# Optimization experiments

Hardware: AMD Instinct MI355X
Metric: run time of the kernel (lower is better)

## Reference

```python
import jax, jax.numpy as jnp
import numpy as np

EPS = 1e-4

@jax.custom_vjp
def bin_active(x):
    # BinActive: sign forward, straight-through (hard-tanh) backward
    return jnp.sign(x)

def _ba_fwd(x):
    return jnp.sign(x), x

def _ba_bwd(x, g):
    return (g * (jnp.abs(x) <= 1.0).astype(g.dtype),)

bin_active.defvjp(_ba_fwd, _ba_bwd)

def norm_bin(x):
    # per-node mean/std (torch .std is unbiased, ddof=1) then binarize
    x = x - jnp.mean(x, axis=1, keepdims=True)
    x = x / (jnp.std(x, axis=1, ddof=1, keepdims=True) + EPS)
    return bin_active(x)

def bin_weight(W):
    # XNOR-style weight binarization: per-output-row scale * sign(W)
    alpha = jnp.mean(jnp.abs(W), axis=1, keepdims=True)
    return alpha * jnp.sign(W)

def bi_sage_conv(x_src, x_tgt, edge_index, W_l, W_r, b):
    # mean-aggregate source messages onto targets, then two binarized linears
    src, dst = edge_index[0], edge_index[1]
    n_tgt = x_tgt.shape[0]
    msg = x_src[src]                                             # [E, F] gather
    agg = jax.ops.segment_sum(msg, dst, num_segments=n_tgt)       # [n_tgt, F]
    cnt = jax.ops.segment_sum(jnp.ones((src.shape[0],), x_src.dtype), dst,
                              num_segments=n_tgt)
    agg = agg / jnp.maximum(cnt, 1.0)[:, None]
    out = agg @ bin_weight(W_l).T + x_tgt @ bin_weight(W_r).T + b
    return out


def setup_inputs() -> dict:
    key = jax.random.key(0)
    ks = jax.random.split(key, 10)
    N0, N1, B = 292864, 11264, 1024
    F_IN, F_HID, F_OUT = 602, 256, 41
    E1, E2 = 281600, 10240
    x = jax.random.normal(ks[0], (N0, F_IN), dtype=jnp.float32)
    # bipartite edges: row0 = source idx in [0, n_src), row1 = target idx in [0, n_tgt)
    ei1 = jnp.stack([jax.random.randint(ks[1], (E1,), 0, N0),
                     jax.random.randint(ks[2], (E1,), 0, N1)]).astype(jnp.int64)
    ei2 = jnp.stack([jax.random.randint(ks[3], (E2,), 0, N1),
                     jax.random.randint(ks[4], (E2,), 0, B)]).astype(jnp.int64)
    s1 = 0.1
    return {
        "x": x,
        "edge_index1": ei1,
        "edge_index2": ei2,
        "n1": N1,
        "n_batch": B,
        "W1_l": s1 * jax.random.normal(ks[5], (F_HID, F_IN), dtype=jnp.float32),
        "W1_r": s1 * jax.random.normal(ks[6], (F_HID, F_IN), dtype=jnp.float32),
        "b1": jnp.zeros((F_HID,), jnp.float32),
        "W2_l": s1 * jax.random.normal(ks[7], (F_OUT, F_HID), dtype=jnp.float32),
        "W2_r": s1 * jax.random.normal(ks[8], (F_OUT, F_HID), dtype=jnp.float32),
        "b2": jnp.zeros((F_OUT,), jnp.float32),
    }


def reference(x, edge_index1, edge_index2, n1, n_batch,
              W1_l, W1_r, b1, W2_l, W2_r, b2):
    # layer 1
    x_t = x[:n1]
    h = bi_sage_conv(norm_bin(x), norm_bin(x_t), edge_index1, W1_l, W1_r, b1)
    h = jax.nn.relu(h)  # dropout p=0.0 -> identity
    # layer 2
    h_t = h[:n_batch]
    out = bi_sage_conv(norm_bin(h), norm_bin(h_t), edge_index2, W2_l, W2_r, b2)
    return jax.nn.log_softmax(out, axis=-1)
```

## Files before the change

kernel.cpp:

```cpp
#include <hip/hip_runtime.h>
#include <hip/hip_bf16.h>
#include <cstdint>
#include <cstddef>

#define CDIV(a,b) (((a)+(b)-1)/(b))

using bf16x8 = __attribute__((ext_vector_type(8))) short;
using f32x4  = __attribute__((ext_vector_type(4))) float;

struct __align__(8) F4 { float x, y, z, w; };
struct __align__(8) F2 { float x, y; };

__device__ __forceinline__ unsigned short sgn_bf16(float s){
  return (s > 0.f) ? 0x3F80u : ((s < 0.f) ? 0xBF80u : 0u);
}

__device__ __forceinline__ int colX(int k){
  int w = k >> 5, b = k & 31;
  if (w < 16){
    int g = w >> 3, wr = w & 7;
    int j = wr >> 1, half = wr & 1;
    return 256*g + 4*(32*half + b) + j;
  }
  int j = w - 16;
  int c = 512 + 4*b + j;
  return (c < 602) ? c : -1;
}
__device__ __forceinline__ int colH(int k){
  int w = k >> 5, b = k & 31;
  int j = w >> 1, half = w & 1;
  return 4*(32*half + b) + j;
}

__device__ __forceinline__ void pack_row602(F4 v0, F4 v1, F4 v2, int lane, uint32_t* pr){
  float s = v0.x+v0.y+v0.z+v0.w + v1.x+v1.y+v1.z+v1.w + v2.x+v2.y+v2.z+v2.w;
  #pragma unroll
  for (int off = 32; off; off >>= 1) s += __shfl_xor(s, off);
  const float mean = s / 602.f;
  uint32_t wpos[20], wneg[20];
  {
    float d0 = v0.x - mean, d1v = v0.y - mean, d2v = v0.z - mean, d3 = v0.w - mean;
    unsigned long long b0 = __ballot(d0 > 0.f), b1 = __ballot(d1v > 0.f),
                       b2 = __ballot(d2v > 0.f), b3 = __ballot(d3 > 0.f);
    wpos[0]=(uint32_t)b0; wpos[1]=(uint32_t)(b0>>32); wpos[2]=(uint32_t)b1; wpos[3]=(uint32_t)(b1>>32);
    wpos[4]=(uint32_t)b2; wpos[5]=(uint32_t)(b2>>32); wpos[6]=(uint32_t)b3; wpos[7]=(uint32_t)(b3>>32);
    b0 = __ballot(d0 < 0.f); b1 = __ballot(d1v < 0.f); b2 = __ballot(d2v < 0.f); b3 = __ballot(d3 < 0.f);
    wneg[0]=(uint32_t)b0; wneg[1]=(uint32_t)(b0>>32); wneg[2]=(uint32_t)b1; wneg[3]=(uint32_t)(b1>>32);
    wneg[4]=(uint32_t)b2; wneg[5]=(uint32_t)(b2>>32); wneg[6]=(uint32_t)b3; wneg[7]=(uint32_t)(b3>>32);
  }
  {
    float d0 = v1.x - mean, d1v = v1.y - mean, d2v = v1.z - mean, d3 = v1.w - mean;
    unsigned long long b0 = __ballot(d0 > 0.f), b1 = __ballot(d1v > 0.f),
                       b2 = __ballot(d2v > 0.f), b3 = __ballot(d3 > 0.f);
    wpos[8]=(uint32_t)b0; wpos[9]=(uint32_t)(b0>>32); wpos[10]=(uint32_t)b1; wpos[11]=(uint32_t)(b1>>32);
    wpos[12]=(uint32_t)b2; wpos[13]=(uint32_t)(b2>>32); wpos[14]=(uint32_t)b3; wpos[15]=(uint32_t)(b3>>32);
    b0 = __ballot(d0 < 0.f); b1 = __ballot(d1v < 0.f); b2 = __ballot(d2v < 0.f); b3 = __ballot(d3 < 0.f);
    wneg[8]=(uint32_t)b0; wneg[9]=(uint32_t)(b0>>32); wneg[10]=(uint32_t)b1; wneg[11]=(uint32_t)(b1>>32);
    wneg[12]=(uint32_t)b2; wneg[13]=(uint32_t)(b2>>32); wneg[14]=(uint32_t)b3; wneg[15]=(uint32_t)(b3>>32);
  }
  {
    int base = 4*lane;
    float d0 = v2.x - mean, d1v = v2.y - mean, d2v = v2.z - mean, d3 = v2.w - mean;
    wpos[16] = (uint32_t)__ballot((base+0 < 90) && (d0 > 0.f));
    wpos[17] = (uint32_t)__ballot((base+1 < 90) && (d1v > 0.f));
    wpos[18] = (uint32_t)__ballot((base+2 < 90) && (d2v > 0.f));
    wpos[19] = (uint32_t)__ballot((base+3 < 90) && (d3 > 0.f));
    wneg[16] = (uint32_t)__ballot((base+0 < 90) && (d0 < 0.f));
    wneg[17] = (uint32_t)__ballot((base+1 < 90) && (d1v < 0.f));
    wneg[18] = (uint32_t)__ballot((base+2 < 90) && (d2v < 0.f));
    wneg[19] = (uint32_t)__ballot((base+3 < 90) && (d3 < 0.f));
  }
  if (lane == 0){
    #pragma unroll
    for (int q = 0; q < 5; ++q){
      uint4 a; a.x = wpos[4*q]; a.y = wpos[4*q+1]; a.z = wpos[4*q+2]; a.w = wpos[4*q+3];
      *(uint4*)&pr[4*q] = a;
      uint4 b; b.x = wneg[4*q]; b.y = wneg[4*q+1]; b.z = wneg[4*q+2]; b.w = wneg[4*q+3];
      *(uint4*)&pr[20 + 4*q] = b;
    }
  }
}

__global__ void prep_all(const float* __restrict__ W1l, const float* __restrict__ W1r,
                         const float* __restrict__ W2l, const float* __restrict__ W2r,
                         float* __restrict__ aL, float* __restrict__ aR,
                         float* __restrict__ a2L, float* __restrict__ a2R,
                         int* __restrict__ degB, int ndeg,
                         unsigned short* __restrict__ bsgn,
                         unsigned char* __restrict__ mask, int n0, int n1){
  int r = blockIdx.x;
  if (r < 594){
    const float* wr; float* dst; int K;
    if (r < 256){ wr = W1l + (size_t)r*602; dst = aL + r; K = 602; }
    else if (r < 512){ int q = r-256; wr = W1r + (size_t)q*602; dst = aR + q; K = 602; }
    else if (r < 553){ int q = r-512; wr = W2l + (size_t)q*256; dst = a2L + q; K = 256; }
    else { int q = r-553; wr = W2r + (size_t)q*256; dst = a2R + q; K = 256; }
    float s = 0.f;
    for (int k = threadIdx.x; k < K; k += blockDim.x) s += fabsf(wr[k]);
    #pragma unroll
    for (int off = 32; off; off >>= 1) s += __shfl_xor(s, off);
    __shared__ float red[4];
    int wid = threadIdx.x >> 6, lane = threadIdx.x & 63;
    if (lane == 0) red[wid] = s;
    __syncthreads();
    if (threadIdx.x == 0) *dst = (red[0]+red[1]+red[2]+red[3]) / (float)K;
  } else if (r < 642){
    int i = (r - 594)*256 + threadIdx.x;
    if (i < ndeg) degB[i] = 0;
  } else if (r < 1922){
    int idx = (r - 642)*256 + threadIdx.x;
    if (idx < 256*1280){
      int o = idx / 1280, k = idx - o*1280;
      float v = 0.f;
      if (k < 640){ int c = colX(k);       if (c >= 0) v = W1l[(size_t)o*602 + c]; }
      else        { int c = colX(k - 640); if (c >= 0) v = W1r[(size_t)o*602 + c]; }
      bsgn[idx] = sgn_bf16(v);
    }
  } else {
    int i = (r - 1922)*256 + threadIdx.x;
    if (i < n0) mask[i] = (i < n1) ? 1 : 0;
  }
}

__global__ void mark_count(const int* __restrict__ s1, const int* __restrict__ d1, int E1,
                           unsigned char* __restrict__ mask, int* __restrict__ deg1,
                           const int* __restrict__ d2, int E2, int* __restrict__ deg2){
  int e = blockIdx.x*blockDim.x + threadIdx.x;
  if (e < E1){
    mask[s1[e]] = 1;
    atomicAdd(&deg1[d1[e]], 1);
  } else if (e < E1 + E2){
    atomicAdd(&deg2[d2[e - E1]], 1);
  }
}

__global__ void pack_scan_bcat(const float* __restrict__ X, uint32_t* __restrict__ P, int nrows,
                               const unsigned char* __restrict__ mask, int packBlocks,
                               const int* __restrict__ deg1, int* __restrict__ rs1, int* __restrict__ cur1, int n1c,
                               const int* __restrict__ deg2, int* __restrict__ rs2, int* __restrict__ cur2, int n2c,
                               const float* __restrict__ W2l, const float* __restrict__ W2r,
                               const float* __restrict__ a2L, const float* __restrict__ a2R,
                               float* __restrict__ Bcat2){
  __shared__ int partial[256];
  const int bid = blockIdx.x;
  if (bid >= packBlocks){
    int role = bid - packBlocks;
    if (role < 2){
      const int* deg = role ? deg2 : deg1;
      int* rs  = role ? rs2  : rs1;
      int* cur = role ? cur2 : cur1;
      int n    = role ? n2c  : n1c;
      int tid = threadIdx.x;
      int per = CDIV(n, 256);
      int begin = tid*per; if (begin > n) begin = n;
      int end = begin + per; if (end > n) end = n;
      int s = 0;
      for (int i = begin; i < end; ++i) s += deg[i];
      partial[tid] = s;
      __syncthreads();
      for (int off = 1; off < 256; off <<= 1){
        int add = (tid >= off) ? partial[tid-off] : 0;
        __syncthreads();
        partial[tid] += add;
        __syncthreads();
      }
      int prefix = (tid == 0) ? 0 : partial[tid-1];
      for (int i = begin; i < end; ++i){ rs[i] = prefix; cur[i] = prefix; prefix += deg[i]; }
      if (tid == 255) rs[n] = prefix;
    } else {
      int idx = (role - 2)*256 + threadIdx.x;
      if (idx < 512*41){
        int o = idx % 41, k = idx / 41;
        int c = (k < 256) ? colH(k) : colH(k - 256);
        float w = (k < 256) ? W2l[(size_t)o*256 + c] : W2r[(size_t)o*256 + c];
        float a = (k < 256) ? a2L[o] : a2R[o];
        float sg = (w > 0.f) ? 1.f : ((w < 0.f) ? -1.f : 0.f);
        Bcat2[idx] = a * sg;
      }
    }
    return;
  }
  const int rp = bid*4 + (threadIdx.x >> 6);
  const int lane = threadIdx.x & 63;
  const int rowA = rp*2, rowB = rp*2 + 1;
  if (rowA >= nrows) return;
  const bool mA = mask[rowA] != 0;
  const bool mB = (rowB < nrows) && (mask[rowB] != 0);
  if (!mA && !mB) return;
  F4 a0 = {0.f,0.f,0.f,0.f}, a1 = a0, a2 = a0;
  F4 c0 = a0, c1 = a0, c2 = a0;
  const float* xa = X + (size_t)rowA * 602;
  const float* xb = X + (size_t)rowB * 602;
  if (mA){
    a0 = *(const F4*)&xa[4*lane];
    a1 = *(const F4*)&xa[256 + 4*lane];
    if (lane < 22) a2 = *(const F4*)&xa[512 + 4*lane];
    else if (lane == 22){ F2 t = *(const F2*)&xa[600]; a2.x = t.x; a2.y = t.y; }
  }
  if (mB){
    c0 = *(const F4*)&xb[4*lane];
    c1 = *(const F4*)&xb[256 + 4*lane];
    if (lane < 22) c2 = *(const F4*)&xb[512 + 4*lane];
    else if (lane == 22){ F2 t = *(const F2*)&xb[600]; c2.x = t.x; c2.y = t.y; }
  }
  if (mA) pack_row602(a0, a1, a2, lane, P + (size_t)rowA * 40);
  if (mB) pack_row602(c0, c1, c2, lane, P + (size_t)rowB * 40);
}

__global__ void fill_both(const int* __restrict__ s1, const int* __restrict__ d1, int E1,
                          int* __restrict__ cur1, int* __restrict__ esrc1,
                          const int* __restrict__ s2, const int* __restrict__ d2, int E2,
                          int* __restrict__ cur2, int* __restrict__ esrc2){
  int e = blockIdx.x*blockDim.x + threadIdx.x;
  if (e < E1){
    int p = atomicAdd(&cur1[d1[e]], 1);
    esrc1[p] = s1[e];
  } else if (e < E1 + E2){
    int q = e - E1;
    int p = atomicAdd(&cur2[d2[q]], 1);
    esrc2[p] = s2[q];
  }
}

__global__ void aggregate_v3(const uint32_t* __restrict__ packed,
                             const int* __restrict__ rs, const int* __restrict__ esrc,
                             unsigned short* __restrict__ S, float* __restrict__ invdeg){
  const int t = blockIdx.x;
  const int lane = threadIdx.x;
  const int slot = lane / 20;
  const int w = lane - slot*20;
  const int s0 = rs[t], s1 = rs[t+1];
  const bool active = slot < 3;
  uint32_t p[8] = {0,0,0,0,0,0,0,0};
  uint32_t n[8] = {0,0,0,0,0,0,0,0};
  for (int base = s0; base < s1; base += 3){
    int e = base + slot;
    uint32_t wp = 0, wn = 0;
    if (active && e < s1){
      const uint32_t* pr = packed + (size_t)esrc[e] * 40;
      wp = pr[w];
      wn = pr[20 + w];
    }
    #pragma unroll
    for (int b = 0; b < 8; ++b){
      p[b] += (wp >> b) & 0x01010101u;
      n[b] += (wn >> b) & 0x01010101u;
    }
  }
  #pragma unroll
  for (int b = 0; b < 8; ++b){
    p[b] += __shfl(p[b], lane + 20) + __shfl(p[b], lane + 40);
    n[b] += __shfl(n[b], lane + 20) + __shfl(n[b], lane + 40);
  }
  if (lane == 0){
    int deg = s1 - s0;
    invdeg[t] = 1.f / (float)(deg > 0 ? deg : 1);
  }
  if (lane < 20){
    unsigned short* sr = S + (size_t)t * 640;
    #pragma unroll
    for (int b = 0; b < 8; ++b){
      #pragma unroll
      for (int k = 0; k < 4; ++k){
        int col = 32*lane + b + 8*k;
        int cnt = (int)((p[b] >> (8*k)) & 0xFF) - (int)((n[b] >> (8*k)) & 0xFF);
        float f = (float)cnt;
        sr[col] = (unsigned short)(__float_as_uint(f) >> 16);
      }
    }
  }
}

__global__ __launch_bounds__(256) void gemm1_fused(
    const unsigned short* __restrict__ Sx, const uint32_t* __restrict__ packedX,
    const unsigned short* __restrict__ bsgn, const float* __restrict__ invdeg,
    const float* __restrict__ aL, const float* __restrict__ aR,
    const float* __restrict__ bias, uint32_t* __restrict__ packedH){
  __shared__ __align__(16) char smem[33792];
  unsigned short (*As)[40] = (unsigned short (*)[40])smem;
  unsigned short (*Bs)[40] = (unsigned short (*)[40])(smem + 32*40*2);
  float (*Hs)[264] = (float (*)[264])smem;

  const int tid = threadIdx.x;
  const int lane = tid & 63, wid = tid >> 6;
  const int m0 = blockIdx.x * 32;
  const int frow = lane & 15, fk = (lane >> 4) * 8;
  const int sRow = tid >> 3, sK = (tid & 7) * 4;

  f32x4 acc1[2][4], acc2[2][4];
  #pragma unroll
  for (int i = 0; i < 2; ++i)
    #pragma unroll
    for (int j = 0; j < 4; ++j){ f32x4 z = {0.f,0.f,0.f,0.f}; acc1[i][j] = z; acc2[i][j] = z; }

  const unsigned short* SxRow = Sx + (size_t)(m0 + sRow) * 640;
  const uint32_t* pxRow = packedX + (size_t)(m0 + sRow) * 40;
  const unsigned short* bsgnCol = bsgn + (size_t)tid * 1280;

  for (int kc = 0; kc < 640; kc += 32){
    *(uint2*)&As[sRow][sK] = *(const uint2*)&SxRow[kc + sK];
    *(bf16x8*)&Bs[tid][0]  = *(const bf16x8*)&bsgnCol[kc];
    *(bf16x8*)&Bs[tid][8]  = *(const bf16x8*)&bsgnCol[kc + 8];
    *(bf16x8*)&Bs[tid][16] = *(const bf16x8*)&bsgnCol[kc + 16];
    *(bf16x8*)&Bs[tid][24] = *(const bf16x8*)&bsgnCol[kc + 24];
    __syncthreads();
    bf16x8 a0 = *(bf16x8*)&As[frow][fk];
    bf16x8 a1 = *(bf16x8*)&As[16 + frow][fk];
    #pragma unroll
    for (int nf = 0; nf < 4; ++nf){
      bf16x8 b = *(bf16x8*)&Bs[wid*64 + nf*16 + frow][fk];
      acc1[0][nf] = __builtin_amdgcn_mfma_f32_16x16x32_bf16(a0, b, acc1[0][nf], 0, 0, 0);
      acc1[1][nf] = __builtin_amdgcn_mfma_f32_16x16x32_bf16(a1, b, acc1[1][nf], 0, 0, 0);
    }
    __syncthreads();
  }
  for (int kc = 0; kc < 640; kc += 32){
    int w = kc >> 5;
    {
      uint32_t wp = pxRow[w];
      uint32_t wq = pxRow[20 + w];
      union { unsigned short u[4]; uint2 v; } tmp;
      #pragma unroll
      for (int j = 0; j < 4; ++j){
        int b_ = sK + j;
        tmp.u[j] = ((wp >> b_) & 1) ? 0x3F80u : (((wq >> b_) & 1) ? 0xBF80u : 0u);
      }
      *(uint2*)&As[sRow][sK] = tmp.v;
    }
    *(bf16x8*)&Bs[tid][0]  = *(const bf16x8*)&bsgnCol[640 + kc];
    *(bf16x8*)&Bs[tid][8]  = *(const bf16x8*)&bsgnCol[640 + kc + 8];
    *(bf16x8*)&Bs[tid][16] = *(const bf16x8*)&bsgnCol[640 + kc + 16];
    *(bf16x8*)&Bs[tid][24] = *(const bf16x8*)&bsgnCol[640 + kc + 24];
    __syncthreads();
    bf16x8 a0 = *(bf16x8*)&As[frow][fk];
    bf16x8 a1 = *(bf16x8*)&As[16 + frow][fk];
    #pragma unroll
    for (int nf = 0; nf < 4; ++nf){
      bf16x8 b = *(bf16x8*)&Bs[wid*64 + nf*16 + frow][fk];
      acc2[0][nf] = __builtin_amdgcn_mfma_f32_16x16x32_bf16(a0, b, acc2[0][nf], 0, 0, 0);
      acc2[1][nf] = __builtin_amdgcn_mfma_f32_16x16x32_bf16(a1, b, acc2[1][nf], 0, 0, 0);
    }
    __syncthreads();
  }

  #pragma unroll
  for (int nf = 0; nf < 4; ++nf){
    int gc = wid*64 + nf*16 + frow;
    float al = aL[gc], ar = aR[gc], bb = bias[gc];
    #pragma unroll
    for (int mf = 0; mf < 2; ++mf){
      #pragma unroll
      for (int reg = 0; reg < 4; ++reg){
        int lr = mf*16 + (lane >> 4)*4 + reg;
        float v = invdeg[m0 + lr]*al*acc1[mf][nf][reg] + ar*acc2[mf][nf][reg] + bb;
        Hs[lr][gc] = fmaxf(v, 0.f);
      }
    }
  }
  __syncthreads();

  for (int r = 0; r < 8; ++r){
    int row = wid*8 + r;
    float4 v = *(const float4*)&Hs[row][4*lane];
    float s = v.x + v.y + v.z + v.w;
    #pragma unroll
    for (int off = 32; off; off >>= 1) s += __shfl_xor(s, off);
    float mean = s * (1.f/256.f);
    float d0 = v.x - mean, d1v = v.y - mean, d2v = v.z - mean, d3 = v.w - mean;
    unsigned long long b0 = __ballot(d0 > 0.f), b1 = __ballot(d1v > 0.f),
                       b2 = __ballot(d2v > 0.f), b3 = __ballot(d3 > 0.f);
    uint32_t wpos[8], wneg[8];
    wpos[0]=(uint32_t)b0; wpos[1]=(uint32_t)(b0>>32); wpos[2]=(uint32_t)b1; wpos[3]=(uint32_t)(b1>>32);
    wpos[4]=(uint32_t)b2; wpos[5]=(uint32_t)(b2>>32); wpos[6]=(uint32_t)b3; wpos[7]=(uint32_t)(b3>>32);
    b0 = __ballot(d0 < 0.f); b1 = __ballot(d1v < 0.f); b2 = __ballot(d2v < 0.f); b3 = __ballot(d3 < 0.f);
    wneg[0]=(uint32_t)b0; wneg[1]=(uint32_t)(b0>>32); wneg[2]=(uint32_t)b1; wneg[3]=(uint32_t)(b1>>32);
    wneg[4]=(uint32_t)b2; wneg[5]=(uint32_t)(b2>>32); wneg[6]=(uint32_t)b3; wneg[7]=(uint32_t)(b3>>32);
    if (lane == 0){
      uint32_t* pr = packedH + (size_t)(m0 + row) * 16;
      *(uint4*)&pr[0]  = make_uint4(wpos[0], wpos[1], wpos[2], wpos[3]);
      *(uint4*)&pr[4]  = make_uint4(wpos[4], wpos[5], wpos[6], wpos[7]);
      *(uint4*)&pr[8]  = make_uint4(wneg[0], wneg[1], wneg[2], wneg[3]);
      *(uint4*)&pr[12] = make_uint4(wneg[4], wneg[5], wneg[6], wneg[7]);
    }
  }
}

__global__ void agg_gemm2(const uint32_t* __restrict__ packedH,
                          const int* __restrict__ rs, const int* __restrict__ esrc,
                          const float* __restrict__ Bcat2, const float* __restrict__ bias,
                          float* __restrict__ out){
  const int t = blockIdx.x;
  const int lane = threadIdx.x;
  const int slot = lane >> 3, w = lane & 7;
  __shared__ float av[512];
  const int s0 = rs[t], s1 = rs[t+1];
  uint32_t p[8] = {0,0,0,0,0,0,0,0};
  uint32_t n[8] = {0,0,0,0,0,0,0,0};
  for (int base = s0; base < s1; base += 8){
    int e = base + slot;
    uint32_t wp = 0, wn = 0;
    if (e < s1){
      const uint32_t* pr = packedH + (size_t)esrc[e] * 16;
      wp = pr[w];
      wn = pr[8 + w];
    }
    #pragma unroll
    for (int b = 0; b < 8; ++b){
      p[b] += (wp >> b) & 0x01010101u;
      n[b] += (wn >> b) & 0x01010101u;
    }
  }
  #pragma unroll
  for (int b = 0; b < 8; ++b){
    p[b] += __shfl_xor(p[b], 8);  p[b] += __shfl_xor(p[b], 16);  p[b] += __shfl_xor(p[b], 32);
    n[b] += __shfl_xor(n[b], 8);  n[b] += __shfl_xor(n[b], 16);  n[b] += __shfl_xor(n[b], 32);
  }
  int deg = s1 - s0;
  float inv = 1.f / (float)(deg > 0 ? deg : 1);
  if (lane < 8){
    #pragma unroll
    for (int b = 0; b < 8; ++b){
      #pragma unroll
      for (int k = 0; k < 4; ++k){
        int col = 32*lane + b + 8*k;
        int cnt = (int)((p[b] >> (8*k)) & 0xFF) - (int)((n[b] >> (8*k)) & 0xFF);
        av[col] = (float)cnt * inv;
      }
    }
  }
  const uint32_t* pr = packedH + (size_t)t * 16;
  for (int k = lane; k < 256; k += 64){
    int wq = k >> 5, b = k & 31;
    av[256 + k] = (float)((pr[wq] >> b) & 1) - (float)((pr[8 + wq] >> b) & 1);
  }
  __syncthreads();
  bool activeO = lane < 41;
  float acc = activeO ? bias[lane] : 0.f;
  for (int k = 0; k < 512; ++k){
    float bw = activeO ? Bcat2[k*41 + lane] : 0.f;
    acc += av[k] * bw;
  }
  float v = activeO ? acc : -INFINITY;
  float m = v;
  #pragma unroll
  for (int off = 32; off; off >>= 1) m = fmaxf(m, __shfl_xor(m, off));
  float e = activeO ? expf(v - m) : 0.f;
  float ssum = e;
  #pragma unroll
  for (int off = 32; off; off >>= 1) ssum += __shfl_xor(ssum, off);
  if (activeO) out[(size_t)t*41 + lane] = v - m - logf(ssum);
}

extern "C" void kernel_launch(void* const* d_in, const int* in_sizes, int n_in,
                              void* d_out, int out_size, void* d_ws, size_t ws_size,
                              hipStream_t stream){
  (void)n_in; (void)out_size; (void)ws_size;
  const float* x   = (const float*)d_in[0];
  const int*   ei1 = (const int*)d_in[1];
  const int*   ei2 = (const int*)d_in[2];
  const float* W1l = (const float*)d_in[5];
  const float* W1r = (const float*)d_in[6];
  const float* b1  = (const float*)d_in[7];
  const float* W2l = (const float*)d_in[8];
  const float* W2r = (const float*)d_in[9];
  const float* b2  = (const float*)d_in[10];
  float* out = (float*)d_out;

  const int FIN = 602, N1 = 11264, NB = 1024;
  const int N0 = in_sizes[0] / FIN;
  const int E1 = in_sizes[1] / 2;
  const int E2 = in_sizes[2] / 2;

  char* wsb = (char*)d_ws;
  size_t off = 0;
  auto carve = [&](size_t bytes)->void*{
    void* p = wsb + off;
    off = (off + bytes + 255) & ~(size_t)255;
    return p;
  };
  uint32_t* packedX = (uint32_t*)carve((size_t)N0*40*4);
  uint32_t* packedH = (uint32_t*)carve((size_t)N1*16*4);
  unsigned short* Sx = (unsigned short*)carve((size_t)N1*640*2);
  float* invdeg1 = (float*)carve((size_t)N1*4);
  unsigned short* bsgn = (unsigned short*)carve((size_t)256*1280*2);
  float* Bcat2 = (float*)carve((size_t)512*41*4);
  float* aL  = (float*)carve(256*4);
  float* aR  = (float*)carve(256*4);
  float* a2L = (float*)carve(64*4);
  float* a2R = (float*)carve(64*4);
  unsigned char* mask = (unsigned char*)carve((size_t)N0);
  int* degB  = (int*)carve((size_t)(N1+NB)*4);
  int* deg1  = degB;
  int* deg2  = degB + N1;
  int* rs1   = (int*)carve((size_t)(N1+1)*4);
  int* cur1  = (int*)carve((size_t)N1*4);
  int* esrc1 = (int*)carve((size_t)E1*4);
  int* rs2   = (int*)carve((size_t)(NB+1)*4);
  int* cur2  = (int*)carve((size_t)NB*4);
  int* esrc2 = (int*)carve((size_t)E2*4);

  const int maskBlocks = CDIV(N0, 256);
  const int cntBlocks  = CDIV(E1 + E2, 256);
  const int packBlocks = CDIV(N0, 8);
  const int bcatBlocks = CDIV(512*41, 256);

  prep_all<<<1922 + maskBlocks, 256, 0, stream>>>(
      W1l, W1r, W2l, W2r, aL, aR, a2L, a2R, degB, N1 + NB, bsgn, mask, N0, N1);
  mark_count<<<cntBlocks, 256, 0, stream>>>(ei1, ei1 + E1, E1, mask, deg1,
                                            ei2 + E2, E2, deg2);
  pack_scan_bcat<<<packBlocks + 2 + bcatBlocks, 256, 0, stream>>>(
      x, packedX, N0, mask, packBlocks,
      deg1, rs1, cur1, N1, deg2, rs2, cur2, NB,
      W2l, W2r, a2L, a2R, Bcat2);
  fill_both<<<cntBlocks, 256, 0, stream>>>(ei1, ei1 + E1, E1, cur1, esrc1,
                                           ei2, ei2 + E2, E2, cur2, esrc2);
  aggregate_v3<<<N1, 64, 0, stream>>>(packedX, rs1, esrc1, Sx, invdeg1);
  gemm1_fused<<<N1/32, 256, 0, stream>>>(Sx, packedX, bsgn, invdeg1, aL, aR, b1, packedH);
  agg_gemm2<<<NB, 64, 0, stream>>>(packedH, rs2, esrc2, Bcat2, b2, out);
}
```

Before: 270.7 us.

## Merge prep and edge-count kernels, memset buffers, register-prefetch GEMM tiles

Folds the edge marking and degree counting into the weight-prep kernel, so one launch does both. The mask and degree buffers are now zeroed with async memsets instead of kernel blocks. The first n1 rows are treated as masked directly in the pack kernel. In gemm1, the next k-chunk of the global A and B operands is loaded into registers before the current chunk's MFMAs run, so global latency overlaps compute. The extra prefetch registers may lower occupancy.

```diff
diff --git a/kernel.cpp b/kernel.cpp
--- a/kernel.cpp
+++ b/kernel.cpp
@@ -81,13 +81,14 @@
   }
 }
 
-__global__ void prep_all(const float* __restrict__ W1l, const float* __restrict__ W1r,
-                         const float* __restrict__ W2l, const float* __restrict__ W2r,
-                         float* __restrict__ aL, float* __restrict__ aR,
-                         float* __restrict__ a2L, float* __restrict__ a2R,
-                         int* __restrict__ degB, int ndeg,
-                         unsigned short* __restrict__ bsgn,
-                         unsigned char* __restrict__ mask, int n0, int n1){
+__global__ void prep_mark(const float* __restrict__ W1l, const float* __restrict__ W1r,
+                          const float* __restrict__ W2l, const float* __restrict__ W2r,
+                          float* __restrict__ aL, float* __restrict__ aR,
+                          float* __restrict__ a2L, float* __restrict__ a2R,
+                          unsigned short* __restrict__ bsgn,
+                          const int* __restrict__ ei1, int E1,
+                          unsigned char* __restrict__ mask, int* __restrict__ deg1,
+                          const int* __restrict__ ei2, int E2, int* __restrict__ deg2){
   int r = blockIdx.x;
   if (r < 594){
     const float* wr; float* dst; int K;
@@ -104,33 +105,22 @@
     if (lane == 0) red[wid] = s;
     __syncthreads();
     if (threadIdx.x == 0) *dst = (red[0]+red[1]+red[2]+red[3]) / (float)K;
-  } else if (r < 642){
-    int i = (r - 594)*256 + threadIdx.x;
-    if (i < ndeg) degB[i] = 0;
-  } else if (r < 1922){
-    int idx = (r - 642)*256 + threadIdx.x;
-    if (idx < 256*1280){
-      int o = idx / 1280, k = idx - o*1280;
-      float v = 0.f;
-      if (k < 640){ int c = colX(k);       if (c >= 0) v = W1l[(size_t)o*602 + c]; }
-      else        { int c = colX(k - 640); if (c >= 0) v = W1r[(size_t)o*602 + c]; }
-      bsgn[idx] = sgn_bf16(v);
-    }
+  } else if (r < 1874){
+    int idx = (r - 594)*256 + threadIdx.x;
+    int o = idx / 1280, k = idx - o*1280;
+    float v = 0.f;
+    if (k < 640){ int c = colX(k);       if (c >= 0) v = W1l[(size_t)o*602 + c]; }
+    else        { int c = colX(k - 640); if (c >= 0) v = W1r[(size_t)o*602 + c]; }
+    bsgn[idx] = sgn_bf16(v);
   } else {
-    int i = (r - 1922)*256 + threadIdx.x;
-    if (i < n0) mask[i] = (i < n1) ? 1 : 0;
-  }
-}
-
-__global__ void mark_count(const int* __restrict__ s1, const int* __restrict__ d1, int E1,
-                           unsigned char* __restrict__ mask, int* __restrict__ deg1,
-                           const int* __restrict__ d2, int E2, int* __restrict__ deg2){
-  int e = blockIdx.x*blockDim.x + threadIdx.x;
-  if (e < E1){
-    mask[s1[e]] = 1;
-    atomicAdd(&deg1[d1[e]], 1);
-  } else if (e < E1 + E2){
-    atomicAdd(&deg2[d2[e - E1]], 1);
+    int e = (r - 1874)*256 + threadIdx.x;
+    if (e < E1){
+      mask[ei1[e]] = 1;
+      atomicAdd(&deg1[ei1[E1 + e]], 1);
+    } else if (e < E1 + E2){
+      int q = e - E1;
+      atomicAdd(&deg2[ei2[E2 + q]], 1);
+    }
   }
 }
 
@@ -184,8 +174,8 @@
   const int lane = threadIdx.x & 63;
   const int rowA = rp*2, rowB = rp*2 + 1;
   if (rowA >= nrows) return;
-  const bool mA = mask[rowA] != 0;
-  const bool mB = (rowB < nrows) && (mask[rowB] != 0);
+  const bool mA = (rowA < n1c) || (mask[rowA] != 0);
+  const bool mB = (rowB < nrows) && ((rowB < n1c) || (mask[rowB] != 0));
   if (!mA && !mB) return;
   F4 a0 = {0.f,0.f,0.f,0.f}, a1 = a0, a2 = a0;
   F4 c0 = a0, c1 = a0, c2 = a0;
@@ -297,13 +287,37 @@
   const uint32_t* pxRow = packedX + (size_t)(m0 + sRow) * 40;
   const unsigned short* bsgnCol = bsgn + (size_t)tid * 1280;
 
+  bf16x8 pb0, pb1, pb2, pb3;
+  uint2 pa;
+  uint32_t pw0 = 0, pw1 = 0;
+
+  pb0 = *(const bf16x8*)&bsgnCol[0];
+  pb1 = *(const bf16x8*)&bsgnCol[8];
+  pb2 = *(const bf16x8*)&bsgnCol[16];
+  pb3 = *(const bf16x8*)&bsgnCol[24];
+  pa  = *(const uint2*)&SxRow[sK];
+
   for (int kc = 0; kc < 640; kc += 32){
-    *(uint2*)&As[sRow][sK] = *(const uint2*)&SxRow[kc + sK];
-    *(bf16x8*)&Bs[tid][0]  = *(const bf16x8*)&bsgnCol[kc];
-    *(bf16x8*)&Bs[tid][8]  = *(const bf16x8*)&bsgnCol[kc + 8];
-    *(bf16x8*)&Bs[tid][16] = *(const bf16x8*)&bsgnCol[kc + 16];
-    *(bf16x8*)&Bs[tid][24] = *(const bf16x8*)&bsgnCol[kc + 24];
+    *(uint2*)&As[sRow][sK] = pa;
+    *(bf16x8*)&Bs[tid][0]  = pb0;
+    *(bf16x8*)&Bs[tid][8]  = pb1;
+    *(bf16x8*)&Bs[tid][16] = pb2;
+    *(bf16x8*)&Bs[tid][24] = pb3;
     __syncthreads();
+    int kn = kc + 32;
+    if (kn < 640){
+      pb0 = *(const bf16x8*)&bsgnCol[kn];
+      pb1 = *(const bf16x8*)&bsgnCol[kn + 8];
+      pb2 = *(const bf16x8*)&bsgnCol[kn + 16];
+      pb3 = *(const bf16x8*)&bsgnCol[kn + 24];
+      pa  = *(const uint2*)&SxRow[kn + sK];
+    } else {
+      pb0 = *(const bf16x8*)&bsgnCol[640];
+      pb1 = *(const bf16x8*)&bsgnCol[648];
+      pb2 = *(const bf16x8*)&bsgnCol[656];
+      pb3 = *(const bf16x8*)&bsgnCol[664];
+      pw0 = pxRow[0]; pw1 = pxRow[20];
+    }
     bf16x8 a0 = *(bf16x8*)&As[frow][fk];
     bf16x8 a1 = *(bf16x8*)&As[16 + frow][fk];
     #pragma unroll
@@ -315,23 +329,29 @@
     __syncthreads();
   }
   for (int kc = 0; kc < 640; kc += 32){
-    int w = kc >> 5;
     {
-      uint32_t wp = pxRow[w];
-      uint32_t wq = pxRow[20 + w];
       union { unsigned short u[4]; uint2 v; } tmp;
       #pragma unroll
       for (int j = 0; j < 4; ++j){
         int b_ = sK + j;
-        tmp.u[j] = ((wp >> b_) & 1) ? 0x3F80u : (((wq >> b_) & 1) ? 0xBF80u : 0u);
+        tmp.u[j] = ((pw0 >> b_) & 1) ? 0x3F80u : (((pw1 >> b_) & 1) ? 0xBF80u : 0u);
       }
       *(uint2*)&As[sRow][sK] = tmp.v;
     }
-    *(bf16x8*)&Bs[tid][0]  = *(const bf16x8*)&bsgnCol[640 + kc];
-    *(bf16x8*)&Bs[tid][8]  = *(const bf16x8*)&bsgnCol[640 + kc + 8];
-    *(bf16x8*)&Bs[tid][16] = *(const bf16x8*)&bsgnCol[640 + kc + 16];
-    *(bf16x8*)&Bs[tid][24] = *(const bf16x8*)&bsgnCol[640 + kc + 24];
+    *(bf16x8*)&Bs[tid][0]  = pb0;
+    *(bf16x8*)&Bs[tid][8]  = pb1;
+    *(bf16x8*)&Bs[tid][16] = pb2;
+    *(bf16x8*)&Bs[tid][24] = pb3;
     __syncthreads();
+    int kn = kc + 32;
+    if (kn < 640){
+      pb0 = *(const bf16x8*)&bsgnCol[640 + kn];
+      pb1 = *(const bf16x8*)&bsgnCol[640 + kn + 8];
+      pb2 = *(const bf16x8*)&bsgnCol[640 + kn + 16];
+      pb3 = *(const bf16x8*)&bsgnCol[640 + kn + 24];
+      int w = kn >> 5;
+      pw0 = pxRow[w]; pw1 = pxRow[20 + w];
+    }
     bf16x8 a0 = *(bf16x8*)&As[frow][fk];
     bf16x8 a1 = *(bf16x8*)&As[16 + frow][fk];
     #pragma unroll
@@ -499,15 +519,15 @@
   int* cur2  = (int*)carve((size_t)NB*4);
   int* esrc2 = (int*)carve((size_t)E2*4);
 
-  const int maskBlocks = CDIV(N0, 256);
   const int cntBlocks  = CDIV(E1 + E2, 256);
   const int packBlocks = CDIV(N0, 8);
   const int bcatBlocks = CDIV(512*41, 256);
 
-  prep_all<<<1922 + maskBlocks, 256, 0, stream>>>(
-      W1l, W1r, W2l, W2r, aL, aR, a2L, a2R, degB, N1 + NB, bsgn, mask, N0, N1);
-  mark_count<<<cntBlocks, 256, 0, stream>>>(ei1, ei1 + E1, E1, mask, deg1,
-                                            ei2 + E2, E2, deg2);
+  hipMemsetAsync(mask, 0, (size_t)N0, stream);
+  hipMemsetAsync(degB, 0, (size_t)(N1+NB)*4, stream);
+  prep_mark<<<1874 + cntBlocks, 256, 0, stream>>>(
+      W1l, W1r, W2l, W2r, aL, aR, a2L, a2R, bsgn,
+      ei1, E1, mask, deg1, ei2, E2, deg2);
   pack_scan_bcat<<<packBlocks + 2 + bcatBlocks, 256, 0, stream>>>(
       x, packedX, N0, mask, packBlocks,
       deg1, rs1, cur1, N1, deg2, rs2, cur2, NB,
```

Result: no change. 274.8 us (+1.5%).
